# Kernel optimization log

Measured on AMD Instinct MI355X. Metric: run time of the kernel, lower is better.

Reference implementation:

```python
import jax, jax.numpy as jnp
import numpy as np

FP8_MAX = 448.0  # max finite value of float8_e4m3fn


def _fp8_quant(v, scale):
    # emulate saturating scaled cast to float8_e4m3fn, then dequant-free fp8 storage (upcast to f32 for the gemm)
    q = jnp.clip(v / scale, -FP8_MAX, FP8_MAX)
    return q.astype(jnp.float8_e4m3fn).astype(jnp.float32)


def setup_inputs() -> dict:
    key = jax.random.key(0)
    k0, k1, k2, k3 = jax.random.split(key, 4)
    T, H, I, E = 1024, 1024, 2816, 8
    x = jax.random.normal(k0, (T, H), jnp.float32)
    router_logits = jax.random.normal(k1, (T, E), jnp.float32)
    w13_weight = jax.random.normal(k2, (E, 2 * I, H), jnp.float32) * 0.02
    w2_weight = jax.random.normal(k3, (E, H, I), jnp.float32) * 0.02
    return {
        "x": x,
        "router_logits": router_logits,
        "w13_weight": w13_weight,
        "w2_weight": w2_weight,
        "w13_input_scale": jnp.ones((E,), jnp.float32),
        "w2_input_scale": jnp.ones((E,), jnp.float32),
        "top_k": 2,
    }


def reference(x, router_logits, w13_weight, w2_weight, w13_input_scale, w2_input_scale, top_k):
    T, H = x.shape
    E, two_I, _ = w13_weight.shape
    I = two_I // 2

    # --- routing: softmax -> top_k -> renormalize (select_experts) ---
    probs = jax.nn.softmax(router_logits, axis=-1)
    topk_w, topk_ids = jax.lax.top_k(probs, top_k)            # [T,K]
    topk_w = topk_w / jnp.sum(topk_w, axis=-1, keepdims=True)
    # dense combine matrix [T,E]: sparsity of the grouped gemm dispatch
    combine = jnp.zeros((T, E), x.dtype).at[jnp.arange(T)[:, None], topk_ids].add(topk_w)

    # --- per-expert fp8 weight quantization (ops.scaled_fp8_quant per expert) ---
    w13_scale = jnp.max(jnp.abs(w13_weight), axis=(1, 2)) / FP8_MAX  # [E]
    w2_scale = jnp.max(jnp.abs(w2_weight), axis=(1, 2)) / FP8_MAX
    w13_q = _fp8_quant(w13_weight, w13_scale[:, None, None])         # [E,2I,H]
    w2_q = _fp8_quant(w2_weight, w2_scale[:, None, None])            # [E,H,I]

    # --- grouped gemm 1: per-expert activation quant + fp8 gemm + dequant scale ---
    x_q = _fp8_quant(x[None], w13_input_scale[:, None, None])        # [E,T,H]
    h = jnp.einsum('eth,eih->eti', x_q, w13_q) * (w13_input_scale * w13_scale)[:, None, None]

    # --- silu_and_mul: gate = first intermediate_size rows, up = second ---
    act = jax.nn.silu(h[..., :I]) * h[..., I:]                       # [E,T,I]

    # --- grouped gemm 2 ---
    act_q = _fp8_quant(act, w2_input_scale[:, None, None])
    o = jnp.einsum('eti,ehi->eth', act_q, w2_q) * (w2_input_scale * w2_scale)[:, None, None]

    # --- post_reorder: weighted combine of selected experts ---
    return jnp.einsum('te,eth->th', combine, o)                      # [T,H]
```

## Files before the change

kernel.cpp:

```cpp
#include <hip/hip_runtime.h>
#include <cstdint>
#include <cstddef>

#define T_TOK 1024
#define H_DIM 1024
#define I_DIM 2816
#define E_NUM 8
#define PAIRS 2048
#define KSPLIT 4
#define NT1 (I_DIM / 32)
#define AMX2_BLKS 128

typedef __attribute__((ext_vector_type(4))) float f32x4;
typedef __attribute__((ext_vector_type(4))) unsigned int u32x4;
typedef long i64;

__device__ __forceinline__ unsigned char fp8e4m3_sw(float v) {
  v = fminf(448.f, fmaxf(-448.f, v));
  unsigned b = __float_as_uint(v);
  unsigned s = (b >> 24) & 0x80u;
  float a = fabsf(v);
  if (a < 0.015625f) {
    int m = (int)rintf(a * 512.f);
    return (unsigned char)(s | (unsigned)m);
  }
  unsigned ab = b & 0x7fffffffu;
  unsigned rnd = 0x7FFFFu + ((ab >> 20) & 1u);
  ab += rnd;
  int e = (int)(ab >> 23) - 127;
  unsigned m = (ab >> 20) & 7u;
  if (e > 8 || (e == 8 && m > 6)) { e = 8; m = 6; }
  return (unsigned char)(s | (unsigned)((e + 7) << 3) | m);
}

__device__ __forceinline__ unsigned q4(float a, float b, float c, float d) {
#if __has_builtin(__builtin_amdgcn_cvt_pk_fp8_f32)
  unsigned w = (unsigned)__builtin_amdgcn_cvt_pk_fp8_f32(a, b, 0, false);
  return (unsigned)__builtin_amdgcn_cvt_pk_fp8_f32(c, d, (int)w, true);
#else
  return (unsigned)fp8e4m3_sw(a) | ((unsigned)fp8e4m3_sw(b) << 8) |
         ((unsigned)fp8e4m3_sw(c) << 16) | ((unsigned)fp8e4m3_sw(d) << 24);
#endif
}

__device__ __forceinline__ unsigned char q1(float a) {
#if __has_builtin(__builtin_amdgcn_cvt_pk_fp8_f32)
  return (unsigned char)((unsigned)__builtin_amdgcn_cvt_pk_fp8_f32(a, a, 0, false) & 0xFFu);
#else
  return fp8e4m3_sw(a);
#endif
}

__device__ __forceinline__ unsigned q4v(float4 f, float inv) {
  return q4(f.x * inv, f.y * inv, f.z * inv, f.w * inv);
}

__global__ __launch_bounds__(1024) void route_k(const float* __restrict__ logits,
                                                unsigned* __restrict__ amax13,
                                                unsigned* __restrict__ amax2,
                                                int* __restrict__ cnt_g,
                                                int* __restrict__ offs_g,
                                                int* __restrict__ pair_tok,
                                                float* __restrict__ pair_w,
                                                int* __restrict__ pairidx) {
  __shared__ int cnt_s[E_NUM], pos_s[E_NUM];
  const int tid = threadIdx.x;
  if (tid < E_NUM) { cnt_s[tid] = 0; amax13[tid] = 0; amax2[tid] = 0; }
  __syncthreads();

  float l[E_NUM];
#pragma unroll
  for (int j = 0; j < E_NUM; j++) l[j] = logits[tid * E_NUM + j];
  int i0 = 0; float b0 = l[0];
#pragma unroll
  for (int j = 1; j < E_NUM; j++) { if (l[j] > b0) { b0 = l[j]; i0 = j; } }
  int i1 = -1; float b1 = -3.4e38f;
#pragma unroll
  for (int j = 0; j < E_NUM; j++) { if (j != i0 && l[j] > b1) { b1 = l[j]; i1 = j; } }
  float e1 = expf(b1 - b0);
  float d = 1.f + e1;
  float w0 = 1.f / d, w1 = e1 / d;

  atomicAdd(&cnt_s[i0], 1);
  atomicAdd(&cnt_s[i1], 1);
  __syncthreads();
  if (tid == 0) {
    int s = 0;
#pragma unroll
    for (int e = 0; e < E_NUM; e++) {
      cnt_g[e] = cnt_s[e];
      offs_g[e] = s;
      pos_s[e] = s;
      s += cnt_s[e];
    }
    offs_g[E_NUM] = s;
  }
  __syncthreads();
  int s0 = atomicAdd(&pos_s[i0], 1);
  pair_tok[s0] = tid; pair_w[s0] = w0; pairidx[2 * tid] = s0;
  int s1 = atomicAdd(&pos_s[i1], 1);
  pair_tok[s1] = tid; pair_w[s1] = w1; pairidx[2 * tid + 1] = s1;
}

__global__ __launch_bounds__(256) void amax13_k(const float* __restrict__ w13,
                                                unsigned* __restrict__ amax13) {
  const int e = blockIdx.y;
  const float4* src = (const float4*)w13 + (size_t)e * (2 * I_DIM * H_DIM / 4);
  int idx = blockIdx.x * 256 + threadIdx.x;
  int stride = gridDim.x * 256;
  float m = 0.f;
#pragma unroll
  for (int j = 0; j < 44; j += 4) {
    float4 v0 = src[idx + (size_t)(j + 0) * stride];
    float4 v1 = src[idx + (size_t)(j + 1) * stride];
    float4 v2 = src[idx + (size_t)(j + 2) * stride];
    float4 v3 = src[idx + (size_t)(j + 3) * stride];
    m = fmaxf(m, fmaxf(fmaxf(fabsf(v0.x), fabsf(v0.y)), fmaxf(fabsf(v0.z), fabsf(v0.w))));
    m = fmaxf(m, fmaxf(fmaxf(fabsf(v1.x), fabsf(v1.y)), fmaxf(fabsf(v1.z), fabsf(v1.w))));
    m = fmaxf(m, fmaxf(fmaxf(fabsf(v2.x), fabsf(v2.y)), fmaxf(fabsf(v2.z), fabsf(v2.w))));
    m = fmaxf(m, fmaxf(fmaxf(fabsf(v3.x), fabsf(v3.y)), fmaxf(fabsf(v3.z), fabsf(v3.w))));
  }
#pragma unroll
  for (int off = 32; off > 0; off >>= 1) m = fmaxf(m, __shfl_xor(m, off));
  __shared__ float wmax[4];
  int lane = threadIdx.x & 63, wid = threadIdx.x >> 6;
  if (lane == 0) wmax[wid] = m;
  __syncthreads();
  if (threadIdx.x == 0) {
    float mm = fmaxf(fmaxf(wmax[0], wmax[1]), fmaxf(wmax[2], wmax[3]));
    atomicMax(&amax13[e], __float_as_uint(mm));
  }
}

__global__ __launch_bounds__(256) void quantx_k(const float* __restrict__ x,
                                                const int* __restrict__ pair_tok,
                                                const int* __restrict__ offs,
                                                const float* __restrict__ s13,
                                                unsigned char* __restrict__ Xq) {
  int p = blockIdx.x;
  int t = pair_tok[p];
  int e = 0;
#pragma unroll
  for (int j = 1; j < E_NUM; j++) { if (p >= offs[j]) e = j; }
  float inv = 1.f / s13[e];
  float4 v = ((const float4*)(x + (size_t)t * H_DIM))[threadIdx.x];
  float a = fminf(448.f, fmaxf(-448.f, v.x * inv));
  float b = fminf(448.f, fmaxf(-448.f, v.y * inv));
  float c = fminf(448.f, fmaxf(-448.f, v.z * inv));
  float dd = fminf(448.f, fmaxf(-448.f, v.w * inv));
  ((unsigned*)(Xq + (size_t)p * H_DIM))[threadIdx.x] = q4(a, b, c, dd);
}

__global__ __launch_bounds__(512) void gemm1_k(const float* __restrict__ w13,
                                               const float* __restrict__ w2,
                                               const unsigned char* __restrict__ Xq,
                                               unsigned char* __restrict__ H1,
                                               const int* __restrict__ cnt,
                                               const int* __restrict__ offs,
                                               const unsigned* __restrict__ amax13,
                                               unsigned* __restrict__ amax2,
                                               const float* __restrict__ s13,
                                               const float* __restrict__ s2in) {
  const int e = blockIdx.z;

  if (blockIdx.x >= NT1) {
    if (blockIdx.y != 0) return;
    const int bx = blockIdx.x - NT1;
    const float4* src = (const float4*)w2 + (size_t)e * (H_DIM * I_DIM / 4);
    int idx = bx * 512 + threadIdx.x;
    int stride = AMX2_BLKS * 512;
    float m = 0.f;
#pragma unroll
    for (int j = 0; j < 11; j++) {
      float4 v = src[idx + (size_t)j * stride];
      m = fmaxf(m, fmaxf(fmaxf(fabsf(v.x), fabsf(v.y)), fmaxf(fabsf(v.z), fabsf(v.w))));
    }
#pragma unroll
    for (int off = 32; off > 0; off >>= 1) m = fmaxf(m, __shfl_xor(m, off));
    __shared__ float wmax2[8];
    int lane = threadIdx.x & 63, wid = threadIdx.x >> 6;
    if (lane == 0) wmax2[wid] = m;
    __syncthreads();
    if (threadIdx.x == 0) {
      float mm = wmax2[0];
#pragma unroll
      for (int j = 1; j < 8; j++) mm = fmaxf(mm, wmax2[j]);
      atomicMax(&amax2[e], __float_as_uint(mm));
    }
    return;
  }

  const int count = cnt[e];
  const int m0 = blockIdx.y * 256;
  if (m0 >= count) return;
  const int nt = blockIdx.x;
  const int base = offs[e];

  const float amax = __uint_as_float(amax13[e]);
  const float inv_w = 448.f / amax;
  const float gs = s13[e] * (amax / 448.f);
  const float inv_a2 = 1.f / s2in[e];

  __shared__ __align__(16) unsigned char As[256][80];
  __shared__ __align__(16) unsigned char Bs[64][80];

  const int tid = threadIdx.x, lane = tid & 63, wq = tid >> 6;
  const int fr = lane & 15, ks = lane >> 4;

  f32x4 accg[2][2], accu[2][2];
#pragma unroll
  for (int i = 0; i < 2; i++)
#pragma unroll
    for (int j = 0; j < 2; j++) { accg[i][j] = (f32x4)0.f; accu[i][j] = (f32x4)0.f; }

  const int ar0 = tid >> 2, ar1 = (tid + 512) >> 2, aseg = tid & 3;
  int pr0 = base + m0 + ar0; if (pr0 > PAIRS - 1) pr0 = PAIRS - 1;
  int pr1 = base + m0 + ar1; if (pr1 > PAIRS - 1) pr1 = PAIRS - 1;
  const unsigned char* a_src0 = Xq + (size_t)pr0 * H_DIM + aseg * 16;
  const unsigned char* a_src1 = Xq + (size_t)pr1 * H_DIM + aseg * 16;

  const int brow = tid >> 3, bseg = tid & 7;
  const size_t brg = (size_t)nt * 32 + (brow & 31) + (size_t)(brow >> 5) * I_DIM;
  const float* b_src = w13 + ((size_t)e * 2 * I_DIM + brg) * H_DIM + bseg * 8;

  u32x4 ra0 = *(const u32x4*)a_src0;
  u32x4 ra1 = *(const u32x4*)a_src1;
  float4 fb0 = ((const float4*)b_src)[0], fb1 = ((const float4*)b_src)[1];
  unsigned qb0 = q4v(fb0, inv_w), qb1 = q4v(fb1, inv_w);

  for (int t = 0; t < H_DIM / 64; ++t) {
    __syncthreads();
    *(u32x4*)&As[ar0][aseg * 16] = ra0;
    *(u32x4*)&As[ar1][aseg * 16] = ra1;
    ((unsigned*)&Bs[brow][bseg * 8])[0] = qb0;
    ((unsigned*)&Bs[brow][bseg * 8])[1] = qb1;
    __syncthreads();
    if (t + 1 < H_DIM / 64) {
      int k0 = (t + 1) * 64;
      ra0 = *(const u32x4*)(a_src0 + k0);
      ra1 = *(const u32x4*)(a_src1 + k0);
      fb0 = ((const float4*)(b_src + k0))[0];
      fb1 = ((const float4*)(b_src + k0))[1];
    }
#pragma unroll
    for (int kk = 0; kk < 2; kk++) {
      i64 a0 = *(const i64*)&As[wq * 32 + fr][kk * 32 + ks * 8];
      i64 a1 = *(const i64*)&As[wq * 32 + 16 + fr][kk * 32 + ks * 8];
#pragma unroll
      for (int ni = 0; ni < 2; ni++) {
        i64 bg = *(const i64*)&Bs[ni * 16 + fr][kk * 32 + ks * 8];
        i64 bu = *(const i64*)&Bs[32 + ni * 16 + fr][kk * 32 + ks * 8];
        accg[0][ni] = __builtin_amdgcn_mfma_f32_16x16x32_fp8_fp8(a0, bg, accg[0][ni], 0, 0, 0);
        accg[1][ni] = __builtin_amdgcn_mfma_f32_16x16x32_fp8_fp8(a1, bg, accg[1][ni], 0, 0, 0);
        accu[0][ni] = __builtin_amdgcn_mfma_f32_16x16x32_fp8_fp8(a0, bu, accu[0][ni], 0, 0, 0);
        accu[1][ni] = __builtin_amdgcn_mfma_f32_16x16x32_fp8_fp8(a1, bu, accu[1][ni], 0, 0, 0);
      }
    }
    qb0 = q4v(fb0, inv_w);
    qb1 = q4v(fb1, inv_w);
  }

  const int rg = lane >> 4;
#pragma unroll
  for (int mi = 0; mi < 2; mi++) {
#pragma unroll
    for (int rr = 0; rr < 4; rr++) {
      int lrow = wq * 32 + mi * 16 + rg * 4 + rr;
      if (m0 + lrow < count) {
        size_t p = (size_t)(base + m0 + lrow);
#pragma unroll
        for (int ni = 0; ni < 2; ni++) {
          int col = nt * 32 + ni * 16 + fr;
          float g = accg[mi][ni][rr] * gs;
          float u = accu[mi][ni][rr] * gs;
          float act = g / (1.f + expf(-g)) * u * inv_a2;
          act = fminf(448.f, fmaxf(-448.f, act));
          H1[p * I_DIM + col] = q1(act);
        }
      }
    }
  }
}

__global__ __launch_bounds__(512) void gemm2_k(const float* __restrict__ w2,
                                               const unsigned char* __restrict__ H1,
                                               float* __restrict__ Op,
                                               const int* __restrict__ cnt,
                                               const int* __restrict__ offs,
                                               const unsigned* __restrict__ amax2,
                                               const float* __restrict__ s2in,
                                               const float* __restrict__ pair_w) {
  const int e = blockIdx.z;
  const int count = cnt[e];
  const int m0 = blockIdx.y * 128;
  if (m0 >= count) return;
  const int nt = blockIdx.x & 15;
  const int ksp = blockIdx.x >> 4;
  const int n0 = nt * 64;
  const int base = offs[e];

  const float amax = __uint_as_float(amax2[e]);
  const float inv_w = 448.f / amax;
  const float s2 = s2in[e] * (amax / 448.f);

  __shared__ __align__(16) unsigned char As[128][80];
  __shared__ __align__(16) unsigned char Bs[64][80];

  const int tid = threadIdx.x, lane = tid & 63, wq = tid >> 6;
  const int fr = lane & 15, ks = lane >> 4;

  f32x4 acc[4];
#pragma unroll
  for (int i = 0; i < 4; i++) acc[i] = (f32x4)0.f;

  const int arow = tid >> 2, aseg = tid & 3;
  int pr = base + m0 + arow; if (pr > PAIRS - 1) pr = PAIRS - 1;
  const unsigned char* a_src = H1 + (size_t)pr * I_DIM + aseg * 16;

  const int brow = tid >> 3, bseg = tid & 7;
  const float* b_src = w2 + ((size_t)e * H_DIM + n0 + brow) * I_DIM + bseg * 8;

  const int KITER = (I_DIM / 64) / KSPLIT;
  const int kbase = ksp * KITER * 64;

  u32x4 ra = *(const u32x4*)(a_src + kbase);
  float4 fb0 = ((const float4*)(b_src + kbase))[0];
  float4 fb1 = ((const float4*)(b_src + kbase))[1];
  unsigned qb0 = q4v(fb0, inv_w), qb1 = q4v(fb1, inv_w);

  for (int t = 0; t < KITER; ++t) {
    __syncthreads();
    *(u32x4*)&As[arow][aseg * 16] = ra;
    ((unsigned*)&Bs[brow][bseg * 8])[0] = qb0;
    ((unsigned*)&Bs[brow][bseg * 8])[1] = qb1;
    __syncthreads();
    if (t + 1 < KITER) {
      int k0 = kbase + (t + 1) * 64;
      ra = *(const u32x4*)(a_src + k0);
      fb0 = ((const float4*)(b_src + k0))[0];
      fb1 = ((const float4*)(b_src + k0))[1];
    }
#pragma unroll
    for (int kk = 0; kk < 2; kk++) {
      i64 a0 = *(const i64*)&As[wq * 16 + fr][kk * 32 + ks * 8];
#pragma unroll
      for (int ni = 0; ni < 4; ni++) {
        i64 b = *(const i64*)&Bs[ni * 16 + fr][kk * 32 + ks * 8];
        acc[ni] = __builtin_amdgcn_mfma_f32_16x16x32_fp8_fp8(a0, b, acc[ni], 0, 0, 0);
      }
    }
    qb0 = q4v(fb0, inv_w);
    qb1 = q4v(fb1, inv_w);
  }

  const int rg = lane >> 4;
#pragma unroll
  for (int rr = 0; rr < 4; rr++) {
    int lrow = wq * 16 + rg * 4 + rr;
    if (m0 + lrow < count) {
      size_t p = (size_t)(base + m0 + lrow);
      float pw = pair_w[p];
#pragma unroll
      for (int ni = 0; ni < 4; ni++) {
        int col = n0 + ni * 16 + fr;
        Op[((size_t)ksp * PAIRS + p) * H_DIM + col] = acc[ni][rr] * s2 * pw;
      }
    }
  }
}

__global__ __launch_bounds__(256) void combine_k(const float* __restrict__ Op,
                                                 const int* __restrict__ pairidx,
                                                 float* __restrict__ out) {
  int t = blockIdx.x;
  int p0 = pairidx[2 * t], p1 = pairidx[2 * t + 1];
  f32x4 acc = (f32x4)0.f;
#pragma unroll
  for (int s = 0; s < KSPLIT; s++) {
    f32x4 a = ((const f32x4*)(Op + ((size_t)s * PAIRS + p0) * H_DIM))[threadIdx.x];
    f32x4 b = ((const f32x4*)(Op + ((size_t)s * PAIRS + p1) * H_DIM))[threadIdx.x];
    acc += a + b;
  }
  ((f32x4*)(out + (size_t)t * H_DIM))[threadIdx.x] = acc;
}

extern "C" void kernel_launch(void* const* d_in, const int* in_sizes, int n_in,
                              void* d_out, int out_size, void* d_ws, size_t ws_size,
                              hipStream_t stream) {
  (void)in_sizes; (void)n_in; (void)out_size; (void)ws_size;
  const float* x      = (const float*)d_in[0];
  const float* logits = (const float*)d_in[1];
  const float* w13    = (const float*)d_in[2];
  const float* w2     = (const float*)d_in[3];
  const float* s13    = (const float*)d_in[4];
  const float* s2in   = (const float*)d_in[5];
  float* out = (float*)d_out;

  char* ws = (char*)d_ws;
  unsigned* amax13 = (unsigned*)(ws + 0);
  unsigned* amax2  = (unsigned*)(ws + 64);
  int* cnt     = (int*)(ws + 128);
  int* offs    = (int*)(ws + 192);
  int* pair_tok = (int*)(ws + 17408);
  float* pair_w = (float*)(ws + 25600);
  int* pairidx  = (int*)(ws + 33792);
  unsigned char* Xq = (unsigned char*)(ws + (size_t)(1 << 20));
  unsigned char* H1 = (unsigned char*)(ws + (size_t)4 * (1 << 20));
  float* Op         = (float*)(ws + (size_t)10 * (1 << 20));

  route_k<<<1, 1024, 0, stream>>>(logits, amax13, amax2, cnt, offs,
                                  pair_tok, pair_w, pairidx);

  amax13_k<<<dim3(128, E_NUM), 256, 0, stream>>>(w13, amax13);

  quantx_k<<<PAIRS, 256, 0, stream>>>(x, pair_tok, offs, s13, Xq);

  gemm1_k<<<dim3(NT1 + AMX2_BLKS, 4, E_NUM), 512, 0, stream>>>(
      w13, w2, Xq, H1, cnt, offs, amax13, amax2, s13, s2in);

  gemm2_k<<<dim3(16 * KSPLIT, 8, E_NUM), 512, 0, stream>>>(
      w2, H1, Op, cnt, offs, amax2, s2in, pair_w);

  combine_k<<<T_TOK, 256, 0, stream>>>(Op, pairidx, out);
}
```

Before: 165.4 us.

## Fuse routing with w13 amax, drop atomics, narrow gemm1 tiles, double-buffer gemm2

Merges the routing kernel and the w13 absmax kernel into one launch. Per-block partial maxima are written to a buffer and reduced inside each gemm block instead of using atomicMax on zeroed globals. gemm1 now uses 16-column tiles with a smaller B tile, doubling the block count, and the w2 amax work is spread over all y-blocks. gemm2 gets a double-buffered LDS pipeline with one barrier per k-step. The aim is to cut launch overhead, improve parallelism and overlap loads with MFMA, at the cost of redundant per-block reductions and lower reuse of A tiles in gemm1.

```diff
diff --git a/kernel.cpp b/kernel.cpp
--- a/kernel.cpp
+++ b/kernel.cpp
@@ -8,8 +8,8 @@
 #define E_NUM 8
 #define PAIRS 2048
 #define KSPLIT 4
-#define NT1 (I_DIM / 32)
-#define AMX2_BLKS 128
+#define NT1 (I_DIM / 16)
+#define AMX2_X 32
 
 typedef __attribute__((ext_vector_type(4))) float f32x4;
 typedef __attribute__((ext_vector_type(4))) unsigned int u32x4;
@@ -55,34 +55,71 @@
   return q4(f.x * inv, f.y * inv, f.z * inv, f.w * inv);
 }
 
-__global__ __launch_bounds__(1024) void route_k(const float* __restrict__ logits,
-                                                unsigned* __restrict__ amax13,
-                                                unsigned* __restrict__ amax2,
-                                                int* __restrict__ cnt_g,
-                                                int* __restrict__ offs_g,
-                                                int* __restrict__ pair_tok,
-                                                float* __restrict__ pair_w,
-                                                int* __restrict__ pairidx) {
+__device__ __forceinline__ float wave_max(float m) {
+#pragma unroll
+  for (int off = 32; off > 0; off >>= 1) m = fmaxf(m, __shfl_xor(m, off));
+  return m;
+}
+
+__global__ __launch_bounds__(256) void pre_k(const float* __restrict__ w13,
+                                             const float* __restrict__ logits,
+                                             float* __restrict__ part13,
+                                             int* __restrict__ cnt_g,
+                                             int* __restrict__ offs_g,
+                                             int* __restrict__ pair_tok,
+                                             float* __restrict__ pair_w,
+                                             int* __restrict__ pairidx) {
+  const int tid = threadIdx.x;
+  if (blockIdx.x < 1024) {
+    const int e = blockIdx.x >> 7, sub = blockIdx.x & 127;
+    const float4* src = (const float4*)w13 + (size_t)e * (2 * I_DIM * H_DIM / 4);
+    int idx = sub * 256 + tid;
+    const int stride = 128 * 256;
+    float m = 0.f;
+#pragma unroll
+    for (int j = 0; j < 44; j += 4) {
+      float4 v0 = src[idx + (size_t)(j + 0) * stride];
+      float4 v1 = src[idx + (size_t)(j + 1) * stride];
+      float4 v2 = src[idx + (size_t)(j + 2) * stride];
+      float4 v3 = src[idx + (size_t)(j + 3) * stride];
+      m = fmaxf(m, fmaxf(fmaxf(fabsf(v0.x), fabsf(v0.y)), fmaxf(fabsf(v0.z), fabsf(v0.w))));
+      m = fmaxf(m, fmaxf(fmaxf(fabsf(v1.x), fabsf(v1.y)), fmaxf(fabsf(v1.z), fabsf(v1.w))));
+      m = fmaxf(m, fmaxf(fmaxf(fabsf(v2.x), fabsf(v2.y)), fmaxf(fabsf(v2.z), fabsf(v2.w))));
+      m = fmaxf(m, fmaxf(fmaxf(fabsf(v3.x), fabsf(v3.y)), fmaxf(fabsf(v3.z), fabsf(v3.w))));
+    }
+    m = wave_max(m);
+    __shared__ float wmax[4];
+    int lane = tid & 63, wid = tid >> 6;
+    if (lane == 0) wmax[wid] = m;
+    __syncthreads();
+    if (tid == 0)
+      part13[blockIdx.x] = fmaxf(fmaxf(wmax[0], wmax[1]), fmaxf(wmax[2], wmax[3]));
+    return;
+  }
+
   __shared__ int cnt_s[E_NUM], pos_s[E_NUM];
-  const int tid = threadIdx.x;
-  if (tid < E_NUM) { cnt_s[tid] = 0; amax13[tid] = 0; amax2[tid] = 0; }
-  __syncthreads();
-
-  float l[E_NUM];
-#pragma unroll
-  for (int j = 0; j < E_NUM; j++) l[j] = logits[tid * E_NUM + j];
-  int i0 = 0; float b0 = l[0];
-#pragma unroll
-  for (int j = 1; j < E_NUM; j++) { if (l[j] > b0) { b0 = l[j]; i0 = j; } }
-  int i1 = -1; float b1 = -3.4e38f;
-#pragma unroll
-  for (int j = 0; j < E_NUM; j++) { if (j != i0 && l[j] > b1) { b1 = l[j]; i1 = j; } }
-  float e1 = expf(b1 - b0);
-  float d = 1.f + e1;
-  float w0 = 1.f / d, w1 = e1 / d;
-
-  atomicAdd(&cnt_s[i0], 1);
-  atomicAdd(&cnt_s[i1], 1);
+  if (tid < E_NUM) cnt_s[tid] = 0;
+  __syncthreads();
+  int i0s[4], i1s[4];
+  float w0s[4], w1s[4];
+#pragma unroll
+  for (int j = 0; j < 4; j++) {
+    int t = tid * 4 + j;
+    float l[E_NUM];
+#pragma unroll
+    for (int k = 0; k < E_NUM; k++) l[k] = logits[t * E_NUM + k];
+    int i0 = 0; float b0 = l[0];
+#pragma unroll
+    for (int k = 1; k < E_NUM; k++) { if (l[k] > b0) { b0 = l[k]; i0 = k; } }
+    int i1 = -1; float b1 = -3.4e38f;
+#pragma unroll
+    for (int k = 0; k < E_NUM; k++) { if (k != i0 && l[k] > b1) { b1 = l[k]; i1 = k; } }
+    float e1 = expf(b1 - b0);
+    float d = 1.f + e1;
+    i0s[j] = i0; i1s[j] = i1; w0s[j] = 1.f / d; w1s[j] = e1 / d;
+    atomicAdd(&cnt_s[i0], 1);
+    atomicAdd(&cnt_s[i1], 1);
+  }
   __syncthreads();
   if (tid == 0) {
     int s = 0;
@@ -96,39 +133,13 @@
     offs_g[E_NUM] = s;
   }
   __syncthreads();
-  int s0 = atomicAdd(&pos_s[i0], 1);
-  pair_tok[s0] = tid; pair_w[s0] = w0; pairidx[2 * tid] = s0;
-  int s1 = atomicAdd(&pos_s[i1], 1);
-  pair_tok[s1] = tid; pair_w[s1] = w1; pairidx[2 * tid + 1] = s1;
-}
-
-__global__ __launch_bounds__(256) void amax13_k(const float* __restrict__ w13,
-                                                unsigned* __restrict__ amax13) {
-  const int e = blockIdx.y;
-  const float4* src = (const float4*)w13 + (size_t)e * (2 * I_DIM * H_DIM / 4);
-  int idx = blockIdx.x * 256 + threadIdx.x;
-  int stride = gridDim.x * 256;
-  float m = 0.f;
-#pragma unroll
-  for (int j = 0; j < 44; j += 4) {
-    float4 v0 = src[idx + (size_t)(j + 0) * stride];
-    float4 v1 = src[idx + (size_t)(j + 1) * stride];
-    float4 v2 = src[idx + (size_t)(j + 2) * stride];
-    float4 v3 = src[idx + (size_t)(j + 3) * stride];
-    m = fmaxf(m, fmaxf(fmaxf(fabsf(v0.x), fabsf(v0.y)), fmaxf(fabsf(v0.z), fabsf(v0.w))));
-    m = fmaxf(m, fmaxf(fmaxf(fabsf(v1.x), fabsf(v1.y)), fmaxf(fabsf(v1.z), fabsf(v1.w))));
-    m = fmaxf(m, fmaxf(fmaxf(fabsf(v2.x), fabsf(v2.y)), fmaxf(fabsf(v2.z), fabsf(v2.w))));
-    m = fmaxf(m, fmaxf(fmaxf(fabsf(v3.x), fabsf(v3.y)), fmaxf(fabsf(v3.z), fabsf(v3.w))));
-  }
-#pragma unroll
-  for (int off = 32; off > 0; off >>= 1) m = fmaxf(m, __shfl_xor(m, off));
-  __shared__ float wmax[4];
-  int lane = threadIdx.x & 63, wid = threadIdx.x >> 6;
-  if (lane == 0) wmax[wid] = m;
-  __syncthreads();
-  if (threadIdx.x == 0) {
-    float mm = fmaxf(fmaxf(wmax[0], wmax[1]), fmaxf(wmax[2], wmax[3]));
-    atomicMax(&amax13[e], __float_as_uint(mm));
+#pragma unroll
+  for (int j = 0; j < 4; j++) {
+    int t = tid * 4 + j;
+    int s0 = atomicAdd(&pos_s[i0s[j]], 1);
+    pair_tok[s0] = t; pair_w[s0] = w0s[j]; pairidx[2 * t] = s0;
+    int s1 = atomicAdd(&pos_s[i1s[j]], 1);
+    pair_tok[s1] = t; pair_w[s1] = w1s[j]; pairidx[2 * t + 1] = s1;
   }
 }
 
@@ -157,38 +168,47 @@
                                                unsigned char* __restrict__ H1,
                                                const int* __restrict__ cnt,
                                                const int* __restrict__ offs,
-                                               const unsigned* __restrict__ amax13,
-                                               unsigned* __restrict__ amax2,
+                                               const float* __restrict__ part13,
+                                               float* __restrict__ part2,
                                                const float* __restrict__ s13,
                                                const float* __restrict__ s2in) {
   const int e = blockIdx.z;
+  const int tid = threadIdx.x, lane = tid & 63, wq = tid >> 6;
 
   if (blockIdx.x >= NT1) {
-    if (blockIdx.y != 0) return;
-    const int bx = blockIdx.x - NT1;
+    const int bx2 = (blockIdx.x - NT1) * 4 + blockIdx.y;
     const float4* src = (const float4*)w2 + (size_t)e * (H_DIM * I_DIM / 4);
-    int idx = bx * 512 + threadIdx.x;
-    int stride = AMX2_BLKS * 512;
+    int idx = bx2 * 512 + tid;
+    const int stride = 128 * 512;
     float m = 0.f;
 #pragma unroll
     for (int j = 0; j < 11; j++) {
       float4 v = src[idx + (size_t)j * stride];
       m = fmaxf(m, fmaxf(fmaxf(fabsf(v.x), fabsf(v.y)), fmaxf(fabsf(v.z), fabsf(v.w))));
     }
-#pragma unroll
-    for (int off = 32; off > 0; off >>= 1) m = fmaxf(m, __shfl_xor(m, off));
+    m = wave_max(m);
     __shared__ float wmax2[8];
-    int lane = threadIdx.x & 63, wid = threadIdx.x >> 6;
-    if (lane == 0) wmax2[wid] = m;
+    if (lane == 0) wmax2[wq] = m;
     __syncthreads();
-    if (threadIdx.x == 0) {
+    if (tid == 0) {
       float mm = wmax2[0];
 #pragma unroll
       for (int j = 1; j < 8; j++) mm = fmaxf(mm, wmax2[j]);
-      atomicMax(&amax2[e], __float_as_uint(mm));
+      part2[e * 128 + bx2] = mm;
     }
     return;
   }
+
+  __shared__ float redA[8];
+  {
+    float v = part13[e * 128 + (tid & 127)];
+    v = wave_max(v);
+    if (lane == 0) redA[wq] = v;
+  }
+  __syncthreads();
+  float amax = redA[0];
+#pragma unroll
+  for (int j = 1; j < 8; j++) amax = fmaxf(amax, redA[j]);
 
   const int count = cnt[e];
   const int m0 = blockIdx.y * 256;
@@ -196,68 +216,58 @@
   const int nt = blockIdx.x;
   const int base = offs[e];
 
-  const float amax = __uint_as_float(amax13[e]);
   const float inv_w = 448.f / amax;
   const float gs = s13[e] * (amax / 448.f);
   const float inv_a2 = 1.f / s2in[e];
 
   __shared__ __align__(16) unsigned char As[256][80];
-  __shared__ __align__(16) unsigned char Bs[64][80];
-
-  const int tid = threadIdx.x, lane = tid & 63, wq = tid >> 6;
+  __shared__ __align__(16) unsigned char Bs[32][80];
+
   const int fr = lane & 15, ks = lane >> 4;
 
-  f32x4 accg[2][2], accu[2][2];
-#pragma unroll
-  for (int i = 0; i < 2; i++)
-#pragma unroll
-    for (int j = 0; j < 2; j++) { accg[i][j] = (f32x4)0.f; accu[i][j] = (f32x4)0.f; }
-
-  const int ar0 = tid >> 2, ar1 = (tid + 512) >> 2, aseg = tid & 3;
-  int pr0 = base + m0 + ar0; if (pr0 > PAIRS - 1) pr0 = PAIRS - 1;
-  int pr1 = base + m0 + ar1; if (pr1 > PAIRS - 1) pr1 = PAIRS - 1;
+  f32x4 accg[2], accu[2];
+#pragma unroll
+  for (int i = 0; i < 2; i++) { accg[i] = (f32x4)0.f; accu[i] = (f32x4)0.f; }
+
+  const int ar0 = tid >> 2, aseg = tid & 3;
+  int pr0 = base + m0 + ar0;       if (pr0 > PAIRS - 1) pr0 = PAIRS - 1;
+  int pr1 = base + m0 + ar0 + 128; if (pr1 > PAIRS - 1) pr1 = PAIRS - 1;
   const unsigned char* a_src0 = Xq + (size_t)pr0 * H_DIM + aseg * 16;
   const unsigned char* a_src1 = Xq + (size_t)pr1 * H_DIM + aseg * 16;
 
-  const int brow = tid >> 3, bseg = tid & 7;
-  const size_t brg = (size_t)nt * 32 + (brow & 31) + (size_t)(brow >> 5) * I_DIM;
-  const float* b_src = w13 + ((size_t)e * 2 * I_DIM + brg) * H_DIM + bseg * 8;
+  const int brow = tid >> 4, bseg = tid & 15;
+  const float* b_src = w13 + ((size_t)e * 2 * I_DIM + (size_t)nt * 16 +
+                              (brow & 15) + (size_t)(brow >> 4) * I_DIM) * H_DIM + bseg * 4;
 
   u32x4 ra0 = *(const u32x4*)a_src0;
   u32x4 ra1 = *(const u32x4*)a_src1;
-  float4 fb0 = ((const float4*)b_src)[0], fb1 = ((const float4*)b_src)[1];
-  unsigned qb0 = q4v(fb0, inv_w), qb1 = q4v(fb1, inv_w);
+  float4 fb = ((const float4*)b_src)[0];
+  unsigned qb = q4v(fb, inv_w);
 
   for (int t = 0; t < H_DIM / 64; ++t) {
     __syncthreads();
     *(u32x4*)&As[ar0][aseg * 16] = ra0;
-    *(u32x4*)&As[ar1][aseg * 16] = ra1;
-    ((unsigned*)&Bs[brow][bseg * 8])[0] = qb0;
-    ((unsigned*)&Bs[brow][bseg * 8])[1] = qb1;
+    *(u32x4*)&As[ar0 + 128][aseg * 16] = ra1;
+    *(unsigned*)&Bs[brow][bseg * 4] = qb;
     __syncthreads();
     if (t + 1 < H_DIM / 64) {
       int k0 = (t + 1) * 64;
       ra0 = *(const u32x4*)(a_src0 + k0);
       ra1 = *(const u32x4*)(a_src1 + k0);
-      fb0 = ((const float4*)(b_src + k0))[0];
-      fb1 = ((const float4*)(b_src + k0))[1];
+      fb = *(const float4*)(b_src + k0);
     }
 #pragma unroll
     for (int kk = 0; kk < 2; kk++) {
       i64 a0 = *(const i64*)&As[wq * 32 + fr][kk * 32 + ks * 8];
       i64 a1 = *(const i64*)&As[wq * 32 + 16 + fr][kk * 32 + ks * 8];
-#pragma unroll
-      for (int ni = 0; ni < 2; ni++) {
-        i64 bg = *(const i64*)&Bs[ni * 16 + fr][kk * 32 + ks * 8];
-        i64 bu = *(const i64*)&Bs[32 + ni * 16 + fr][kk * 32 + ks * 8];
-        accg[0][ni] = __builtin_amdgcn_mfma_f32_16x16x32_fp8_fp8(a0, bg, accg[0][ni], 0, 0, 0);
-        accg[1][ni] = __builtin_amdgcn_mfma_f32_16x16x32_fp8_fp8(a1, bg, accg[1][ni], 0, 0, 0);
-        accu[0][ni] = __builtin_amdgcn_mfma_f32_16x16x32_fp8_fp8(a0, bu, accu[0][ni], 0, 0, 0);
-        accu[1][ni] = __builtin_amdgcn_mfma_f32_16x16x32_fp8_fp8(a1, bu, accu[1][ni], 0, 0, 0);
-      }
-    }
-    qb0 = q4v(fb0, inv_w);
-    qb1 = q4v(fb1, inv_w);
+      i64 bg = *(const i64*)&Bs[fr][kk * 32 + ks * 8];
+      i64 bu = *(const i64*)&Bs[16 + fr][kk * 32 + ks * 8];
+      accg[0] = __builtin_amdgcn_mfma_f32_16x16x32_fp8_fp8(a0, bg, accg[0], 0, 0, 0);
+      accg[1] = __builtin_amdgcn_mfma_f32_16x16x32_fp8_fp8(a1, bg, accg[1], 0, 0, 0);
+      accu[0] = __builtin_amdgcn_mfma_f32_16x16x32_fp8_fp8(a0, bu, accu[0], 0, 0, 0);
+      accu[1] = __builtin_amdgcn_mfma_f32_16x16x32_fp8_fp8(a1, bu, accu[1], 0, 0, 0);
+    }
+    qb = q4v(fb, inv_w);
   }
 
   const int rg = lane >> 4;
@@ -268,15 +278,12 @@
       int lrow = wq * 32 + mi * 16 + rg * 4 + rr;
       if (m0 + lrow < count) {
         size_t p = (size_t)(base + m0 + lrow);
-#pragma unroll
-        for (int ni = 0; ni < 2; ni++) {
-          int col = nt * 32 + ni * 16 + fr;
-          float g = accg[mi][ni][rr] * gs;
-          float u = accu[mi][ni][rr] * gs;
-          float act = g / (1.f + expf(-g)) * u * inv_a2;
-          act = fminf(448.f, fmaxf(-448.f, act));
-          H1[p * I_DIM + col] = q1(act);
-        }
+        int col = nt * 16 + fr;
+        float g = accg[mi][rr] * gs;
+        float u = accu[mi][rr] * gs;
+        float act = g / (1.f + expf(-g)) * u * inv_a2;
+        act = fminf(448.f, fmaxf(-448.f, act));
+        H1[p * I_DIM + col] = q1(act);
       }
     }
   }
@@ -287,10 +294,23 @@
                                                float* __restrict__ Op,
                                                const int* __restrict__ cnt,
                                                const int* __restrict__ offs,
-                                               const unsigned* __restrict__ amax2,
+                                               const float* __restrict__ part2,
                                                const float* __restrict__ s2in,
                                                const float* __restrict__ pair_w) {
   const int e = blockIdx.z;
+  const int tid = threadIdx.x, lane = tid & 63, wq = tid >> 6;
+
+  __shared__ float redA[8];
+  {
+    float v = part2[e * 128 + (tid & 127)];
+    v = wave_max(v);
+    if (lane == 0) redA[wq] = v;
+  }
+  __syncthreads();
+  float amax = redA[0];
+#pragma unroll
+  for (int j = 1; j < 8; j++) amax = fmaxf(amax, redA[j]);
+
   const int count = cnt[e];
   const int m0 = blockIdx.y * 128;
   if (m0 >= count) return;
@@ -299,14 +319,12 @@
   const int n0 = nt * 64;
   const int base = offs[e];
 
-  const float amax = __uint_as_float(amax2[e]);
   const float inv_w = 448.f / amax;
   const float s2 = s2in[e] * (amax / 448.f);
 
-  __shared__ __align__(16) unsigned char As[128][80];
-  __shared__ __align__(16) unsigned char Bs[64][80];
-
-  const int tid = threadIdx.x, lane = tid & 63, wq = tid >> 6;
+  __shared__ __align__(16) unsigned char As[2][128][80];
+  __shared__ __align__(16) unsigned char Bs[2][64][80];
+
   const int fr = lane & 15, ks = lane >> 4;
 
   f32x4 acc[4];
@@ -326,31 +344,45 @@
   u32x4 ra = *(const u32x4*)(a_src + kbase);
   float4 fb0 = ((const float4*)(b_src + kbase))[0];
   float4 fb1 = ((const float4*)(b_src + kbase))[1];
-  unsigned qb0 = q4v(fb0, inv_w), qb1 = q4v(fb1, inv_w);
-
+  {
+    unsigned qb0 = q4v(fb0, inv_w), qb1 = q4v(fb1, inv_w);
+    *(u32x4*)&As[0][arow][aseg * 16] = ra;
+    ((unsigned*)&Bs[0][brow][bseg * 8])[0] = qb0;
+    ((unsigned*)&Bs[0][brow][bseg * 8])[1] = qb1;
+  }
+  {
+    int k0 = kbase + 64;
+    ra = *(const u32x4*)(a_src + k0);
+    fb0 = ((const float4*)(b_src + k0))[0];
+    fb1 = ((const float4*)(b_src + k0))[1];
+  }
+  __syncthreads();
+
+  int c = 0;
   for (int t = 0; t < KITER; ++t) {
-    __syncthreads();
-    *(u32x4*)&As[arow][aseg * 16] = ra;
-    ((unsigned*)&Bs[brow][bseg * 8])[0] = qb0;
-    ((unsigned*)&Bs[brow][bseg * 8])[1] = qb1;
-    __syncthreads();
+#pragma unroll
+    for (int kk = 0; kk < 2; kk++) {
+      i64 a0 = *(const i64*)&As[c][wq * 16 + fr][kk * 32 + ks * 8];
+#pragma unroll
+      for (int ni = 0; ni < 4; ni++) {
+        i64 b = *(const i64*)&Bs[c][ni * 16 + fr][kk * 32 + ks * 8];
+        acc[ni] = __builtin_amdgcn_mfma_f32_16x16x32_fp8_fp8(a0, b, acc[ni], 0, 0, 0);
+      }
+    }
     if (t + 1 < KITER) {
-      int k0 = kbase + (t + 1) * 64;
+      unsigned qb0 = q4v(fb0, inv_w), qb1 = q4v(fb1, inv_w);
+      *(u32x4*)&As[c ^ 1][arow][aseg * 16] = ra;
+      ((unsigned*)&Bs[c ^ 1][brow][bseg * 8])[0] = qb0;
+      ((unsigned*)&Bs[c ^ 1][brow][bseg * 8])[1] = qb1;
+    }
+    if (t + 2 < KITER) {
+      int k0 = kbase + (t + 2) * 64;
       ra = *(const u32x4*)(a_src + k0);
       fb0 = ((const float4*)(b_src + k0))[0];
       fb1 = ((const float4*)(b_src + k0))[1];
     }
-#pragma unroll
-    for (int kk = 0; kk < 2; kk++) {
-      i64 a0 = *(const i64*)&As[wq * 16 + fr][kk * 32 + ks * 8];
-#pragma unroll
-      for (int ni = 0; ni < 4; ni++) {
-        i64 b = *(const i64*)&Bs[ni * 16 + fr][kk * 32 + ks * 8];
-        acc[ni] = __builtin_amdgcn_mfma_f32_16x16x32_fp8_fp8(a0, b, acc[ni], 0, 0, 0);
-      }
-    }
-    qb0 = q4v(fb0, inv_w);
-    qb1 = q4v(fb1, inv_w);
+    __syncthreads();
+    c ^= 1;
   }
 
   const int rg = lane >> 4;
@@ -397,10 +429,10 @@
   float* out = (float*)d_out;
 
   char* ws = (char*)d_ws;
-  unsigned* amax13 = (unsigned*)(ws + 0);
-  unsigned* amax2  = (unsigned*)(ws + 64);
-  int* cnt     = (int*)(ws + 128);
-  int* offs    = (int*)(ws + 192);
+  int* cnt      = (int*)(ws + 128);
+  int* offs     = (int*)(ws + 192);
+  float* part13 = (float*)(ws + 4096);
+  float* part2  = (float*)(ws + 8192);
   int* pair_tok = (int*)(ws + 17408);
   float* pair_w = (float*)(ws + 25600);
   int* pairidx  = (int*)(ws + 33792);
@@ -408,18 +440,16 @@
   unsigned char* H1 = (unsigned char*)(ws + (size_t)4 * (1 << 20));
   float* Op         = (float*)(ws + (size_t)10 * (1 << 20));
 
-  route_k<<<1, 1024, 0, stream>>>(logits, amax13, amax2, cnt, offs,
+  pre_k<<<1025, 256, 0, stream>>>(w13, logits, part13, cnt, offs,
                                   pair_tok, pair_w, pairidx);
 
-  amax13_k<<<dim3(128, E_NUM), 256, 0, stream>>>(w13, amax13);
-
   quantx_k<<<PAIRS, 256, 0, stream>>>(x, pair_tok, offs, s13, Xq);
 
-  gemm1_k<<<dim3(NT1 + AMX2_BLKS, 4, E_NUM), 512, 0, stream>>>(
-      w13, w2, Xq, H1, cnt, offs, amax13, amax2, s13, s2in);
+  gemm1_k<<<dim3(NT1 + AMX2_X, 4, E_NUM), 512, 0, stream>>>(
+      w13, w2, Xq, H1, cnt, offs, part13, part2, s13, s2in);
 
   gemm2_k<<<dim3(16 * KSPLIT, 8, E_NUM), 512, 0, stream>>>(
-      w2, H1, Op, cnt, offs, amax2, s2in, pair_w);
+      w2, H1, Op, cnt, offs, part2, s2in, pair_w);
 
   combine_k<<<T_TOK, 256, 0, stream>>>(Op, pairidx, out);
 }
```

Measured after the change: 173.7 us. 5.0% more time.
